# Kernel optimization log

Measured on AMD Instinct MI355X. Metric: run time of the kernel, lower is better.

## Reference

```python
import jax, jax.numpy as jnp
import numpy as np

B, N_HEADS, DIM, Z, X = 128, 12, 768, 7, 14


def _rpe_index(z, x):
    """2D concatenated self-attention relative positional encoding index.
    Tokens = z*z template tokens followed by x*x search tokens. Two token
    pairs share a bias index iff they have the same (dh, dw, region_i, region_j).
    """
    zh, zw = np.meshgrid(np.arange(z), np.arange(z), indexing='ij')
    xh, xw = np.meshgrid(np.arange(x), np.arange(x), indexing='ij')
    h = np.concatenate([zh.ravel(), xh.ravel()])
    w = np.concatenate([zw.ravel(), xw.ravel()])
    region = np.concatenate([np.zeros(z * z, np.int64), np.ones(x * x, np.int64)])
    dh = h[:, None] - h[None, :]
    dw = w[:, None] - w[None, :]
    rb = np.broadcast_to(region[:, None], dh.shape)
    rc = np.broadcast_to(region[None, :], dh.shape)
    key = np.stack([dh, dw, rb, rc], axis=-1).reshape(-1, 4)
    _, inv = np.unique(key, axis=0, return_inverse=True)
    return inv.reshape(dh.shape)  # (N, N) int


def setup_inputs() -> dict:
    key = jax.random.key(0)
    ks = jax.random.split(key, 4)
    N = Z * Z + X * X  # 245
    idx = _rpe_index(Z, X)
    n_bias = int(idx.max()) + 1
    return {
        "x": jax.random.normal(ks[0], (B, N, DIM), jnp.float32),
        "qkv_w": jax.random.normal(ks[1], (3 * DIM, DIM), jnp.float32) * 0.02,
        "proj_w": jax.random.normal(ks[2], (DIM, DIM), jnp.float32) * 0.02,
        "proj_b": jnp.zeros((DIM,), jnp.float32),
        "bias_table": jax.random.normal(ks[3], (N_HEADS, n_bias), jnp.float32) * 0.02,
        "rel_index": jnp.asarray(idx, jnp.int32),
    }


def reference(x, qkv_w, proj_w, proj_b, bias_table, rel_index):
    Bq, N, C = x.shape
    H = N_HEADS
    Dh = C // H
    scale = Dh ** -0.5
    # qkv projection (no bias): (B, N, 3, H, Dh)
    qkv = (x @ qkv_w.T).reshape(Bq, N, 3, H, Dh)
    q = jnp.moveaxis(qkv[:, :, 0], 2, 1)  # (B, H, N, Dh)
    k = jnp.moveaxis(qkv[:, :, 1], 2, 1)
    v = jnp.moveaxis(qkv[:, :, 2], 2, 1)
    attn = jnp.einsum('bhnd,bhmd->bhnm', q, k) * scale  # (B, H, N, N)
    # relative position bias gather: (H, N, N) broadcast over batch
    attn = attn + bias_table[:, rel_index][None]
    attn = jax.nn.softmax(attn, axis=-1)
    out = jnp.einsum('bhnm,bhmd->bhnd', attn, v)  # (B, H, N, Dh)
    out = jnp.moveaxis(out, 1, 2).reshape(Bq, N, C)
    return out @ proj_w.T + proj_b
```

## Files before the change

kernel.cpp:

```cpp
#include <hip/hip_runtime.h>
#include <hip/hip_bf16.h>
#include <stdint.h>

#define BATCH 128
#define NTOK 245
#define HEADS 12
#define DHEAD 64
#define CDIM 768
#define KT 24
#define SUBT 512

typedef __attribute__((ext_vector_type(8))) short short8;
typedef __attribute__((ext_vector_type(4))) float f32x4;

__device__ __forceinline__ float bf2f(uint32_t hbits) {
    union { uint32_t u; float f; } v; v.u = hbits << 16; return v.f;
}
__device__ __forceinline__ uint32_t f2bf(float f) {
    union { float f; uint32_t u; } v; v.f = f;
    return (v.u + 0x7fffu + ((v.u >> 16) & 1u)) >> 16;
}
__device__ __forceinline__ ushort2 pk2bf(float x, float y) {
    union { __hip_bfloat162 h; ushort2 u; } c;
    c.h = __float22bfloat162_rn(make_float2(x, y));
    return c.u;
}
__device__ __forceinline__ size_t tiled_addr(int m, int k) {
    return (((size_t)(m >> 4) * KT + (k >> 5)) * 64 + ((k >> 3) & 3) * 16 + (m & 15)) * 8
           + (k & 7);
}
__device__ __forceinline__ void gl_lds16(const uint16_t* g, ushort* lds) {
    __builtin_amdgcn_global_load_lds(
        (const __attribute__((address_space(1))) void*)g,
        (__attribute__((address_space(3))) void*)lds,
        16, 0, 0);
}

__global__ __launch_bounds__(256)
void cvt_tile_bf16(const float* __restrict__ src, uint16_t* __restrict__ dst, int n8)
{
    int i = blockIdx.x * 256 + threadIdx.x;
    const int stride = gridDim.x * 256;
    for (; i < n8; i += stride) {
        const int sl = i & 63;
        const int tile = i >> 6;
        const int rt = tile / KT, kt = tile - rt * KT;
        const size_t soff = (size_t)(rt * 16 + (sl & 15)) * CDIM + kt * 32 + (sl >> 4) * 8;
        float4 a = *(const float4*)(src + soff);
        float4 b = *(const float4*)(src + soff + 4);
        ushort2 p0 = pk2bf(a.x, a.y), p1 = pk2bf(a.z, a.w);
        ushort2 p2 = pk2bf(b.x, b.y), p3 = pk2bf(b.z, b.w);
        uint4 o;
        o.x = (uint32_t)p0.x | ((uint32_t)p0.y << 16);
        o.y = (uint32_t)p1.x | ((uint32_t)p1.y << 16);
        o.z = (uint32_t)p2.x | ((uint32_t)p2.y << 16);
        o.w = (uint32_t)p3.x | ((uint32_t)p3.y << 16);
        *(uint4*)(dst + (size_t)i * 8) = o;
    }
}

__global__ __launch_bounds__(256)
void bias_pre(const float* __restrict__ bias_table, const int* __restrict__ rel,
              int n_bias, uint16_t* __restrict__ bias_t)
{
    const int h = blockIdx.x, j = blockIdx.y, q = threadIdx.x;
    float v = -30000.f;
    if (j < NTOK && q < NTOK) v = bias_table[(size_t)h * n_bias + rel[q * NTOK + j]];
    bias_t[((size_t)h * 256 + j) * 256 + q] = (uint16_t)f2bf(v);
}

#define GEMM_LOOP                                                                \
    gl_lds16(gA0, &Af[0][w  ][0][0]);                                            \
    gl_lds16(gA1, &Af[0][w+4][0][0]);                                            \
    gl_lds16(gB0, &Bf[0][w  ][0][0]);                                            \
    gl_lds16(gB1, &Bf[0][w+4][0][0]);                                            \
    gl_lds16(gA0 + SUBT, &Af[1][w  ][0][0]);                                     \
    gl_lds16(gA1 + SUBT, &Af[1][w+4][0][0]);                                     \
    gl_lds16(gB0 + SUBT, &Bf[1][w  ][0][0]);                                     \
    gl_lds16(gB1 + SUBT, &Bf[1][w+4][0][0]);                                     \
    int cur = 0, nxt = 2;                                                        \
    _Pragma("unroll 1")                                                          \
    for (int t = 0; t < KT; ++t) {                                               \
        if (t == KT - 1) { asm volatile("s_waitcnt vmcnt(0) lgkmcnt(0)" ::: "memory"); } \
        else             { asm volatile("s_waitcnt vmcnt(4) lgkmcnt(0)" ::: "memory"); } \
        __builtin_amdgcn_s_barrier();                                            \
        if (t + 2 < KT) {                                                        \
            const int ko = (t + 2) * SUBT;                                       \
            gl_lds16(gA0 + ko, &Af[nxt][w  ][0][0]);                             \
            gl_lds16(gA1 + ko, &Af[nxt][w+4][0][0]);                             \
            gl_lds16(gB0 + ko, &Bf[nxt][w  ][0][0]);                             \
            gl_lds16(gB1 + ko, &Bf[nxt][w+4][0][0]);                             \
        }                                                                        \
        short8 af[4], bf[4];                                                     \
        _Pragma("unroll")                                                        \
        for (int m = 0; m < 4; ++m)                                              \
            af[m] = *(const short8*)&Af[cur][wr*4 + m][l][0];                    \
        _Pragma("unroll")                                                        \
        for (int n = 0; n < 4; ++n)                                              \
            bf[n] = *(const short8*)&Bf[cur][wc*4 + n][l][0];                    \
        _Pragma("unroll")                                                        \
        for (int m = 0; m < 4; ++m)                                              \
            _Pragma("unroll")                                                    \
            for (int n = 0; n < 4; ++n)                                          \
                acc[m][n] = __builtin_amdgcn_mfma_f32_16x16x32_bf16(bf[n], af[m], acc[m][n], 0, 0, 0); \
        cur = (cur == 2) ? 0 : cur + 1;                                          \
        nxt = (nxt == 2) ? 0 : nxt + 1;                                          \
    }

__global__ __launch_bounds__(256)
void qkv_gemm_mfma(const uint16_t* __restrict__ xb, const uint16_t* __restrict__ wq,
                   uint16_t* __restrict__ qkv)
{
    __shared__ ushort Af[3][8][64][8];
    __shared__ ushort Bf[3][8][64][8];
    const int t = threadIdx.x;
    const int w = t >> 6, l = t & 63;
    const int wr = w >> 1, wc = w & 1;
    const int lm = l & 15, lk = l >> 4;

    const int bid = blockIdx.x;
    const int xcd = bid & 7;
    const int wg = (xcd < 2 ? xcd * 552 : 1104 + (xcd - 2) * 551) + (bid >> 3);
    const int mtile = wg / 18, ctile = wg - mtile * 18;
    const int m0 = mtile * 128, c0 = ctile * 128;

    const uint16_t* gA0 = xb + ((size_t)(mtile*8 + w    ) * KT * 64 + l) * 8;
    const uint16_t* gA1 = xb + ((size_t)(mtile*8 + w + 4) * KT * 64 + l) * 8;
    const uint16_t* gB0 = wq + ((size_t)(ctile*8 + w    ) * KT * 64 + l) * 8;
    const uint16_t* gB1 = wq + ((size_t)(ctile*8 + w + 4) * KT * 64 + l) * 8;

    f32x4 acc[4][4];
    #pragma unroll
    for (int m = 0; m < 4; ++m)
        #pragma unroll
        for (int n = 0; n < 4; ++n) acc[m][n] = (f32x4){0.f,0.f,0.f,0.f};

    GEMM_LOOP

    int sArr[4], hArr[4], dArr[4];
    #pragma unroll
    for (int n = 0; n < 4; ++n) {
        int c = c0 + wc*64 + n*16 + lk*4;
        int s = c / CDIM; int rem = c - s * CDIM;
        sArr[n] = s; hArr[n] = rem >> 6; dArr[n] = rem & 63;
    }
    #pragma unroll
    for (int m = 0; m < 4; ++m) {
        int gm  = m0 + wr*64 + m*16 + lm;
        int b   = gm / NTOK;
        int tok = gm - b * NTOK;
        #pragma unroll
        for (int n = 0; n < 4; ++n) {
            ushort2 u0 = pk2bf(acc[m][n][0], acc[m][n][1]);
            ushort2 u1 = pk2bf(acc[m][n][2], acc[m][n][3]);
            uint2 pk;
            pk.x = (uint32_t)u0.x | ((uint32_t)u0.y << 16);
            pk.y = (uint32_t)u1.x | ((uint32_t)u1.y << 16);
            size_t addr = ((((size_t)b*3 + sArr[n])*HEADS + hArr[n])*NTOK + tok)*DHEAD + dArr[n];
            *(uint2*)(qkv + addr) = pk;
        }
    }
}

__global__ __launch_bounds__(512)
void attn_mfma(const uint16_t* __restrict__ qkv, const uint16_t* __restrict__ bias_t,
               uint16_t* __restrict__ o_t)
{
    __shared__ ushort Ks[256][72];
    __shared__ ushort Vt[64][264];
    __shared__ ushort Ps[8][16][72];
    const int bh = blockIdx.x;
    const int b = bh / HEADS, h = bh % HEADS;
    const int t = threadIdx.x;
    const int w = t >> 6, l = t & 63;
    const int lm = l & 15, lk = l >> 4;
    const int wq0 = w * 32;

    const uint16_t* qbase = qkv + (((size_t)b*3 + 0)*HEADS + h) * (NTOK*DHEAD);
    const uint16_t* kbase = qkv + (((size_t)b*3 + 1)*HEADS + h) * (NTOK*DHEAD);
    const uint16_t* vbase = qkv + (((size_t)b*3 + 2)*HEADS + h) * (NTOK*DHEAD);
    const uint16_t* btab  = bias_t + (size_t)h * 256 * 256;

    {
        const int col = (t & 7) * 8;
        #pragma unroll
        for (int p = 0; p < 4; ++p) {
            int row = p * 64 + (t >> 3);
            uint4 val = make_uint4(0u,0u,0u,0u);
            if (row < NTOK) val = *(const uint4*)(kbase + (size_t)row * DHEAD + col);
            *(uint4*)&Ks[row][col] = val;
        }
    }
    {
        const int j  = t >> 1;
        const int dh = (t & 1) * 32;
        uint4 r0 = make_uint4(0,0,0,0), r1 = r0, r2 = r0, r3 = r0;
        if (j < NTOK) {
            const uint16_t* src = vbase + (size_t)j * DHEAD + dh;
            r0 = *(const uint4*)(src);
            r1 = *(const uint4*)(src + 8);
            r2 = *(const uint4*)(src + 16);
            r3 = *(const uint4*)(src + 24);
        }
        union { uint4 v[4]; ushort s[32]; } u;
        u.v[0] = r0; u.v[1] = r1; u.v[2] = r2; u.v[3] = r3;
        #pragma unroll
        for (int i = 0; i < 32; ++i)
            Vt[dh + i][j] = u.s[i];
    }

    short8 qf[2][2];
    #pragma unroll
    for (int m = 0; m < 2; ++m) {
        int qrow = wq0 + m*16 + lm; if (qrow > NTOK-1) qrow = NTOK-1;
        #pragma unroll
        for (int k2 = 0; k2 < 2; ++k2)
            qf[m][k2] = *(const short8*)(qbase + (size_t)qrow * DHEAD + k2*32 + lk*8);
    }

    f32x4 acc_o[2][4];
    float lsum[2][4];
    #pragma unroll
    for (int m = 0; m < 2; ++m) {
        #pragma unroll
        for (int n = 0; n < 4; ++n) acc_o[m][n] = (f32x4){0.f,0.f,0.f,0.f};
        #pragma unroll
        for (int r = 0; r < 4; ++r) lsum[m][r] = 0.f;
    }

    __syncthreads();

    for (int jb = 0; jb < 4; ++jb) {
        short8 kf[4][2], vf[4][2];
        #pragma unroll
        for (int n = 0; n < 4; ++n)
            #pragma unroll
            for (int k2 = 0; k2 < 2; ++k2) {
                kf[n][k2] = *(const short8*)&Ks[jb*64 + n*16 + lm][k2*32 + lk*8];
                vf[n][k2] = *(const short8*)&Vt[n*16 + lm][jb*64 + k2*32 + lk*8];
            }

        #pragma unroll
        for (int m = 0; m < 2; ++m) {
            f32x4 sv[4];
            #pragma unroll
            for (int n = 0; n < 4; ++n) {
                f32x4 z = (f32x4){0.f,0.f,0.f,0.f};
                sv[n] = __builtin_amdgcn_mfma_f32_16x16x32_bf16(qf[m][0], kf[n][0], z, 0, 0, 0);
                sv[n] = __builtin_amdgcn_mfma_f32_16x16x32_bf16(qf[m][1], kf[n][1], sv[n], 0, 0, 0);
            }
            #pragma unroll
            for (int n = 0; n < 4; ++n) {
                uint2 bb = *(const uint2*)(btab + (size_t)(jb*64 + n*16 + lm) * 256 + wq0 + m*16 + lk*4);
                float s0 = fmaf(sv[n][0], 0.125f, bf2f(bb.x & 0xffffu));
                float s1 = fmaf(sv[n][1], 0.125f, bf2f(bb.x >> 16));
                float s2 = fmaf(sv[n][2], 0.125f, bf2f(bb.y & 0xffffu));
                float s3 = fmaf(sv[n][3], 0.125f, bf2f(bb.y >> 16));
                sv[n][0] = __expf(fminf(s0, 30.f));
                sv[n][1] = __expf(fminf(s1, 30.f));
                sv[n][2] = __expf(fminf(s2, 30.f));
                sv[n][3] = __expf(fminf(s3, 30.f));
            }
            #pragma unroll
            for (int n = 0; n < 4; ++n)
                #pragma unroll
                for (int r = 0; r < 4; ++r) {
                    ushort u = (ushort)f2bf(sv[n][r]);
                    lsum[m][r] += bf2f(u);
                    Ps[w][lk*4 + r][n*16 + lm] = u;
                }
            short8 pf[2];
            #pragma unroll
            for (int k2 = 0; k2 < 2; ++k2)
                pf[k2] = *(const short8*)&Ps[w][lm][k2*32 + lk*8];
            #pragma unroll
            for (int n = 0; n < 4; ++n) {
                acc_o[m][n] = __builtin_amdgcn_mfma_f32_16x16x32_bf16(pf[0], vf[n][0], acc_o[m][n], 0, 0, 0);
                acc_o[m][n] = __builtin_amdgcn_mfma_f32_16x16x32_bf16(pf[1], vf[n][1], acc_o[m][n], 0, 0, 0);
            }
        }
    }

    #pragma unroll
    for (int m = 0; m < 2; ++m) {
        float inv[4];
        #pragma unroll
        for (int r = 0; r < 4; ++r) {
            float s = lsum[m][r];
            s += __shfl_xor(s, 1);
            s += __shfl_xor(s, 2);
            s += __shfl_xor(s, 4);
            s += __shfl_xor(s, 8);
            inv[r] = 1.f / s;
        }
        #pragma unroll
        for (int r = 0; r < 4; ++r) {
            int q = wq0 + m*16 + lk*4 + r;
            if (q < NTOK) {
                int gm = b * NTOK + q;
                #pragma unroll
                for (int n = 0; n < 4; ++n) {
                    int k = h * DHEAD + n*16 + lm;
                    o_t[tiled_addr(gm, k)] = (uint16_t)f2bf(acc_o[m][n][r] * inv[r]);
                }
            }
        }
    }
}

__global__ __launch_bounds__(256)
void proj_gemm_mfma(const uint16_t* __restrict__ ot, const uint16_t* __restrict__ wp,
                    const float* __restrict__ bias, float* __restrict__ out)
{
    __shared__ ushort Af[3][8][64][8];
    __shared__ ushort Bf[3][8][64][8];
    const int t = threadIdx.x;
    const int w = t >> 6, l = t & 63;
    const int wr = w >> 1, wc = w & 1;
    const int lm = l & 15, lk = l >> 4;

    const int bid = blockIdx.x;
    const int xcd = bid & 7;
    const int wg = (xcd < 6 ? xcd * 184 : 1104 + (xcd - 6) * 183) + (bid >> 3);
    const int mtile = wg / 6, ctile = wg - mtile * 6;
    const int m0 = mtile * 128, c0 = ctile * 128;

    const uint16_t* gA0 = ot + ((size_t)(mtile*8 + w    ) * KT * 64 + l) * 8;
    const uint16_t* gA1 = ot + ((size_t)(mtile*8 + w + 4) * KT * 64 + l) * 8;
    const uint16_t* gB0 = wp + ((size_t)(ctile*8 + w    ) * KT * 64 + l) * 8;
    const uint16_t* gB1 = wp + ((size_t)(ctile*8 + w + 4) * KT * 64 + l) * 8;

    f32x4 acc[4][4];
    #pragma unroll
    for (int m = 0; m < 4; ++m)
        #pragma unroll
        for (int n = 0; n < 4; ++n) acc[m][n] = (f32x4){0.f,0.f,0.f,0.f};

    GEMM_LOOP

    float4 bsv[4]; int cArr[4];
    #pragma unroll
    for (int n = 0; n < 4; ++n) {
        cArr[n] = c0 + wc*64 + n*16 + lk*4;
        bsv[n]  = *(const float4*)(bias + cArr[n]);
    }
    #pragma unroll
    for (int m = 0; m < 4; ++m) {
        int gm = m0 + wr*64 + m*16 + lm;
        #pragma unroll
        for (int n = 0; n < 4; ++n) {
            float4 r;
            r.x = acc[m][n][0] + bsv[n].x;
            r.y = acc[m][n][1] + bsv[n].y;
            r.z = acc[m][n][2] + bsv[n].z;
            r.w = acc[m][n][3] + bsv[n].w;
            *(float4*)(out + (size_t)gm * CDIM + cArr[n]) = r;
        }
    }
}

extern "C" void kernel_launch(void* const* d_in, const int* in_sizes, int n_in,
                              void* d_out, int out_size, void* d_ws, size_t ws_size,
                              hipStream_t stream)
{
    (void)n_in; (void)out_size;
    const float* x          = (const float*)d_in[0];
    const float* qkv_w      = (const float*)d_in[1];
    const float* proj_w     = (const float*)d_in[2];
    const float* proj_b     = (const float*)d_in[3];
    const float* bias_table = (const float*)d_in[4];
    const int*   rel        = (const int*)d_in[5];
    const int n_bias = in_sizes[4] / HEADS;

    const size_t qkv_elems = (size_t)BATCH * 3 * HEADS * NTOK * DHEAD;
    const size_t o_elems   = (size_t)BATCH * HEADS * NTOK * DHEAD;
    const size_t bt_elems  = (size_t)HEADS * 256 * 256;
    const size_t wq_elems  = (size_t)3 * CDIM * CDIM;
    const size_t wp_elems  = (size_t)CDIM * CDIM;

    uint16_t* qkv_ws = (uint16_t*)d_ws;
    uint16_t* o_ws   = qkv_ws + qkv_elems;
    uint16_t* bt_ws  = o_ws + o_elems;
    uint16_t* wq_ws  = bt_ws + bt_elems;
    uint16_t* wp_ws  = wq_ws + wq_elems;
    const size_t need = (qkv_elems + o_elems + bt_elems + wq_elems + wp_elems) * sizeof(uint16_t);
    if (ws_size < need) return;

    uint16_t* xb = o_ws;

    cvt_tile_bf16<<<2048, 256, 0, stream>>>(x, xb, (int)(o_elems / 8));
    cvt_tile_bf16<<<864, 256, 0, stream>>>(qkv_w, wq_ws, (int)(wq_elems / 8));
    cvt_tile_bf16<<<288, 256, 0, stream>>>(proj_w, wp_ws, (int)(wp_elems / 8));

    bias_pre<<<dim3(HEADS, 256), 256, 0, stream>>>(bias_table, rel, n_bias, bt_ws);

    qkv_gemm_mfma<<<4410, 256, 0, stream>>>(xb, wq_ws, qkv_ws);

    attn_mfma<<<dim3(BATCH * HEADS), 512, 0, stream>>>(qkv_ws, bt_ws, o_ws);

    proj_gemm_mfma<<<1470, 256, 0, stream>>>(o_ws, wp_ws, proj_b, (float*)d_out);
}
```

Before: 322.1 us.

## Stream K/V in two halves to cut LDS, fold log2e into bias, use exp2

The attention kernel now loads K and V into LDS in two 128-token halves rather than all 256 tokens at once, roughly halving shared memory per block so more blocks can be resident per CU. The bias table is premultiplied by log2(e) and the score scale is changed to match, so the softmax exponent uses exp2f directly. It also adds s_setprio around the MFMA sections and uses a hardware bf16 pack for the probabilities. In exchange each block does an extra reload and barrier round, and the pad value and clamp are rescaled to the base-2 domain.

Measured after the change: 332.8 us. +3.3%, slower.

```diff
diff --git a/kernel.cpp b/kernel.cpp
--- a/kernel.cpp
+++ b/kernel.cpp
@@ -1,6 +1,7 @@
 #include <hip/hip_runtime.h>
 #include <hip/hip_bf16.h>
 #include <stdint.h>
+#include <math.h>
 
 #define BATCH 128
 #define NTOK 245
@@ -9,6 +10,8 @@
 #define CDIM 768
 #define KT 24
 #define SUBT 512
+#define SCL 0.18033688f
+#define PCLAMP 43.3f
 
 typedef __attribute__((ext_vector_type(8))) short short8;
 typedef __attribute__((ext_vector_type(4))) float f32x4;
@@ -64,8 +67,9 @@
               int n_bias, uint16_t* __restrict__ bias_t)
 {
     const int h = blockIdx.x, j = blockIdx.y, q = threadIdx.x;
-    float v = -30000.f;
-    if (j < NTOK && q < NTOK) v = bias_table[(size_t)h * n_bias + rel[q * NTOK + j]];
+    float v = -43281.f;
+    if (j < NTOK && q < NTOK)
+        v = bias_table[(size_t)h * n_bias + rel[q * NTOK + j]] * 1.44269504f;
     bias_t[((size_t)h * 256 + j) * 256 + q] = (uint16_t)f2bf(v);
 }
 
@@ -166,8 +170,8 @@
 void attn_mfma(const uint16_t* __restrict__ qkv, const uint16_t* __restrict__ bias_t,
                uint16_t* __restrict__ o_t)
 {
-    __shared__ ushort Ks[256][72];
-    __shared__ ushort Vt[64][264];
+    __shared__ ushort Ks[128][72];
+    __shared__ ushort Vt[64][136];
     __shared__ ushort Ps[8][16][72];
     const int bh = blockIdx.x;
     const int b = bh / HEADS, h = bh % HEADS;
@@ -181,34 +185,6 @@
     const uint16_t* vbase = qkv + (((size_t)b*3 + 2)*HEADS + h) * (NTOK*DHEAD);
     const uint16_t* btab  = bias_t + (size_t)h * 256 * 256;
 
-    {
-        const int col = (t & 7) * 8;
-        #pragma unroll
-        for (int p = 0; p < 4; ++p) {
-            int row = p * 64 + (t >> 3);
-            uint4 val = make_uint4(0u,0u,0u,0u);
-            if (row < NTOK) val = *(const uint4*)(kbase + (size_t)row * DHEAD + col);
-            *(uint4*)&Ks[row][col] = val;
-        }
-    }
-    {
-        const int j  = t >> 1;
-        const int dh = (t & 1) * 32;
-        uint4 r0 = make_uint4(0,0,0,0), r1 = r0, r2 = r0, r3 = r0;
-        if (j < NTOK) {
-            const uint16_t* src = vbase + (size_t)j * DHEAD + dh;
-            r0 = *(const uint4*)(src);
-            r1 = *(const uint4*)(src + 8);
-            r2 = *(const uint4*)(src + 16);
-            r3 = *(const uint4*)(src + 24);
-        }
-        union { uint4 v[4]; ushort s[32]; } u;
-        u.v[0] = r0; u.v[1] = r1; u.v[2] = r2; u.v[3] = r3;
-        #pragma unroll
-        for (int i = 0; i < 32; ++i)
-            Vt[dh + i][j] = u.s[i];
-    }
-
     short8 qf[2][2];
     #pragma unroll
     for (int m = 0; m < 2; ++m) {
@@ -228,57 +204,93 @@
         for (int r = 0; r < 4; ++r) lsum[m][r] = 0.f;
     }
 
-    __syncthreads();
-
-    for (int jb = 0; jb < 4; ++jb) {
-        short8 kf[4][2], vf[4][2];
-        #pragma unroll
-        for (int n = 0; n < 4; ++n)
+    for (int kh = 0; kh < 2; ++kh) {
+        {
+            const int col = (t & 7) * 8;
             #pragma unroll
-            for (int k2 = 0; k2 < 2; ++k2) {
-                kf[n][k2] = *(const short8*)&Ks[jb*64 + n*16 + lm][k2*32 + lk*8];
-                vf[n][k2] = *(const short8*)&Vt[n*16 + lm][jb*64 + k2*32 + lk*8];
+            for (int p = 0; p < 2; ++p) {
+                int rloc = p * 64 + (t >> 3);
+                int row = kh * 128 + rloc;
+                uint4 val = make_uint4(0u,0u,0u,0u);
+                if (row < NTOK) val = *(const uint4*)(kbase + (size_t)row * DHEAD + col);
+                *(uint4*)&Ks[rloc][col] = val;
             }
-
-        #pragma unroll
-        for (int m = 0; m < 2; ++m) {
-            f32x4 sv[4];
+        }
+        {
+            const int jloc = t >> 2;
+            const int j = kh * 128 + jloc;
+            const int dh = (t & 3) * 16;
+            uint4 r0 = make_uint4(0,0,0,0), r1 = r0;
+            if (j < NTOK) {
+                const uint16_t* src = vbase + (size_t)j * DHEAD + dh;
+                r0 = *(const uint4*)(src);
+                r1 = *(const uint4*)(src + 8);
+            }
+            union { uint4 v[2]; ushort s[16]; } u;
+            u.v[0] = r0; u.v[1] = r1;
             #pragma unroll
-            for (int n = 0; n < 4; ++n) {
-                f32x4 z = (f32x4){0.f,0.f,0.f,0.f};
-                sv[n] = __builtin_amdgcn_mfma_f32_16x16x32_bf16(qf[m][0], kf[n][0], z, 0, 0, 0);
-                sv[n] = __builtin_amdgcn_mfma_f32_16x16x32_bf16(qf[m][1], kf[n][1], sv[n], 0, 0, 0);
-            }
-            #pragma unroll
-            for (int n = 0; n < 4; ++n) {
-                uint2 bb = *(const uint2*)(btab + (size_t)(jb*64 + n*16 + lm) * 256 + wq0 + m*16 + lk*4);
-                float s0 = fmaf(sv[n][0], 0.125f, bf2f(bb.x & 0xffffu));
-                float s1 = fmaf(sv[n][1], 0.125f, bf2f(bb.x >> 16));
-                float s2 = fmaf(sv[n][2], 0.125f, bf2f(bb.y & 0xffffu));
-                float s3 = fmaf(sv[n][3], 0.125f, bf2f(bb.y >> 16));
-                sv[n][0] = __expf(fminf(s0, 30.f));
-                sv[n][1] = __expf(fminf(s1, 30.f));
-                sv[n][2] = __expf(fminf(s2, 30.f));
-                sv[n][3] = __expf(fminf(s3, 30.f));
-            }
+            for (int i = 0; i < 16; ++i)
+                Vt[dh + i][jloc] = u.s[i];
+        }
+        __syncthreads();
+
+        #pragma unroll
+        for (int jb2 = 0; jb2 < 2; ++jb2) {
+            short8 kf[4][2], vf[4][2];
             #pragma unroll
             for (int n = 0; n < 4; ++n)
                 #pragma unroll
-                for (int r = 0; r < 4; ++r) {
-                    ushort u = (ushort)f2bf(sv[n][r]);
-                    lsum[m][r] += bf2f(u);
-                    Ps[w][lk*4 + r][n*16 + lm] = u;
+                for (int k2 = 0; k2 < 2; ++k2) {
+                    kf[n][k2] = *(const short8*)&Ks[jb2*64 + n*16 + lm][k2*32 + lk*8];
+                    vf[n][k2] = *(const short8*)&Vt[n*16 + lm][jb2*64 + k2*32 + lk*8];
                 }
-            short8 pf[2];
+            const int jbg = kh * 2 + jb2;
+
             #pragma unroll
-            for (int k2 = 0; k2 < 2; ++k2)
-                pf[k2] = *(const short8*)&Ps[w][lm][k2*32 + lk*8];
-            #pragma unroll
-            for (int n = 0; n < 4; ++n) {
-                acc_o[m][n] = __builtin_amdgcn_mfma_f32_16x16x32_bf16(pf[0], vf[n][0], acc_o[m][n], 0, 0, 0);
-                acc_o[m][n] = __builtin_amdgcn_mfma_f32_16x16x32_bf16(pf[1], vf[n][1], acc_o[m][n], 0, 0, 0);
+            for (int m = 0; m < 2; ++m) {
+                f32x4 sv[4];
+                __builtin_amdgcn_s_setprio(1);
+                #pragma unroll
+                for (int n = 0; n < 4; ++n) {
+                    f32x4 z = (f32x4){0.f,0.f,0.f,0.f};
+                    sv[n] = __builtin_amdgcn_mfma_f32_16x16x32_bf16(qf[m][0], kf[n][0], z, 0, 0, 0);
+                    sv[n] = __builtin_amdgcn_mfma_f32_16x16x32_bf16(qf[m][1], kf[n][1], sv[n], 0, 0, 0);
+                }
+                __builtin_amdgcn_s_setprio(0);
+                #pragma unroll
+                for (int n = 0; n < 4; ++n) {
+                    uint2 bb = *(const uint2*)(btab + (size_t)(jbg*64 + n*16 + lm) * 256 + wq0 + m*16 + lk*4);
+                    float s0 = fmaf(sv[n][0], SCL, bf2f(bb.x & 0xffffu));
+                    float s1 = fmaf(sv[n][1], SCL, bf2f(bb.x >> 16));
+                    float s2 = fmaf(sv[n][2], SCL, bf2f(bb.y & 0xffffu));
+                    float s3 = fmaf(sv[n][3], SCL, bf2f(bb.y >> 16));
+                    sv[n][0] = exp2f(fminf(s0, PCLAMP));
+                    sv[n][1] = exp2f(fminf(s1, PCLAMP));
+                    sv[n][2] = exp2f(fminf(s2, PCLAMP));
+                    sv[n][3] = exp2f(fminf(s3, PCLAMP));
+                }
+                #pragma unroll
+                for (int n = 0; n < 4; ++n)
+                    #pragma unroll
+                    for (int r = 0; r < 4; ++r) {
+                        ushort u = pk2bf(sv[n][r], sv[n][r]).x;
+                        lsum[m][r] += bf2f(u);
+                        Ps[w][lk*4 + r][n*16 + lm] = u;
+                    }
+                short8 pf[2];
+                #pragma unroll
+                for (int k2 = 0; k2 < 2; ++k2)
+                    pf[k2] = *(const short8*)&Ps[w][lm][k2*32 + lk*8];
+                __builtin_amdgcn_s_setprio(1);
+                #pragma unroll
+                for (int n = 0; n < 4; ++n) {
+                    acc_o[m][n] = __builtin_amdgcn_mfma_f32_16x16x32_bf16(pf[0], vf[n][0], acc_o[m][n], 0, 0, 0);
+                    acc_o[m][n] = __builtin_amdgcn_mfma_f32_16x16x32_bf16(pf[1], vf[n][1], acc_o[m][n], 0, 0, 0);
+                }
+                __builtin_amdgcn_s_setprio(0);
             }
         }
+        __syncthreads();
     }
 
     #pragma unroll
```
